# Kernel tuning notes

Measured on AMD Instinct MI355X. Metric: run time of the kernel, lower is better.

Reference implementation:

```python
import jax, jax.numpy as jnp
import numpy as np

P = 10      # num_prototypes == embed_dim
H = 2       # num_heads
F = 64      # ffn_dim
L = 2       # transformer_blocks
DH = P // H # head dim = 5


def _layernorm(x, g, b, eps=1e-5):
    mu = jnp.mean(x, axis=-1, keepdims=True)
    var = jnp.var(x, axis=-1, keepdims=True)
    return (x - mu) * jax.lax.rsqrt(var + eps) * g + b


def setup_inputs() -> dict:
    key = jax.random.key(0)
    ks = jax.random.split(key, 16)
    B = 1_000_000
    inp = {
        "x": jax.random.normal(ks[0], (B, 8), dtype=jnp.float32),
        "prototypes": jax.random.normal(ks[1], (P, 8), dtype=jnp.float32),
        # attention projections, stacked over layers
        "Wq": jax.random.normal(ks[2], (L, P, P), dtype=jnp.float32) * 0.1,
        "bq": jnp.zeros((L, P), dtype=jnp.float32),
        "Wk": jax.random.normal(ks[3], (L, P, P), dtype=jnp.float32) * 0.1,
        "bk": jnp.zeros((L, P), dtype=jnp.float32),
        "Wv": jax.random.normal(ks[4], (L, P, P), dtype=jnp.float32) * 0.1,
        "bv": jnp.zeros((L, P), dtype=jnp.float32),
        "Wo": jax.random.normal(ks[5], (L, P, P), dtype=jnp.float32) * 0.1,
        "bo": jnp.zeros((L, P), dtype=jnp.float32),
        "ln1_g": jnp.ones((L, P), dtype=jnp.float32),
        "ln1_b": jnp.zeros((L, P), dtype=jnp.float32),
        "ln2_g": jnp.ones((L, P), dtype=jnp.float32),
        "ln2_b": jnp.zeros((L, P), dtype=jnp.float32),
        # FFN
        "W1": jax.random.normal(ks[6], (L, P, F), dtype=jnp.float32) * 0.1,
        "b1": jnp.zeros((L, F), dtype=jnp.float32),
        "W2": jax.random.normal(ks[7], (L, F, P), dtype=jnp.float32) * 0.1,
        "b2": jnp.zeros((L, P), dtype=jnp.float32),
        # classifier (num_classes=2 -> single logit + sigmoid)
        "Wc": jax.random.normal(ks[8], (P, 1), dtype=jnp.float32) * 0.1,
        "bc": jnp.zeros((1,), dtype=jnp.float32),
    }
    return inp


def _forward(x, prototypes, Wq, bq, Wk, bk, Wv, bv, Wo, bo,
             ln1_g, ln1_b, ln2_g, ln2_b, W1, b1, W2, b2, Wc, bc):
    # ---- vectorized RBF kernel matrix (replaces the B*P python loop) ----
    x2 = jnp.sum(x * x, axis=-1, keepdims=True)            # [B,1]
    p2 = jnp.sum(prototypes * prototypes, axis=-1)          # [P]
    sq = x2 + p2[None, :] - 2.0 * (x @ prototypes.T)        # [B,P]
    km = jnp.exp(-sq)                                       # [B,P] quantum-kernel proxy

    seq = km[:, None, :]                                    # [B, S=1, P]
    scale = 1.0 / jnp.sqrt(jnp.asarray(DH, dtype=seq.dtype))
    B = seq.shape[0]

    for l in range(L):  # small fixed layer count
        # pre-norm multi-head self-attention (seq_len == 1)
        h = _layernorm(seq, ln1_g[l], ln1_b[l])
        q = (h @ Wq[l] + bq[l]).reshape(B, 1, H, DH)
        k = (h @ Wk[l] + bk[l]).reshape(B, 1, H, DH)
        v = (h @ Wv[l] + bv[l]).reshape(B, 1, H, DH)
        scores = jnp.einsum('bqhd,bkhd->bhqk', q, k) * scale
        attn = jax.nn.softmax(scores, axis=-1)
        o = jnp.einsum('bhqk,bkhd->bqhd', attn, v).reshape(B, 1, P)
        seq = seq + (o @ Wo[l] + bo[l])
        # pre-norm FFN
        h2 = _layernorm(seq, ln2_g[l], ln2_b[l])
        seq = seq + (jax.nn.gelu(h2 @ W1[l] + b1[l]) @ W2[l] + b2[l])

    logits = seq[:, 0, :] @ Wc + bc                          # [B,1]
    return jax.nn.sigmoid(logits)


def reference(x, prototypes, Wq, bq, Wk, bk, Wv, bv, Wo, bo,
              ln1_g, ln1_b, ln2_g, ln2_b, W1, b1, W2, b2, Wc, bc):
    return _forward(x, prototypes, Wq, bq, Wk, bk, Wv, bv, Wo, bo,
                    ln1_g, ln1_b, ln2_g, ln2_b, W1, b1, W2, b2, Wc, bc)
```

## Files before the change

### kernel.cpp

```cpp
#include <hip/hip_runtime.h>
#include <hip/hip_fp16.h>
#include <cmath>

#define PP 10
#define FF 64
#define LL 2
#define BLOCK 256
#define EPT 2
#define L2E 1.44269504088896f

typedef _Float16 h2 __attribute__((ext_vector_type(2)));

struct GeluCoef { float c[5]; };

#define WS_P2L   0
#define WS_MPROT 16
#define WS_M1P   96
#define WS_C1    196
#define WS_FFNU  216
#define WS_W2C   1752
#define WS_HC    1784

__device__ __forceinline__ float fast_sigmoid(float z) {
    return __builtin_amdgcn_rcpf(1.0f + exp2f(-L2E * z));
}

__device__ __forceinline__ unsigned int pack_h2f(float a, float b) {
    _Float16 ha = (_Float16)a, hb = (_Float16)b;
    unsigned short ua = __builtin_bit_cast(unsigned short, ha);
    unsigned short ub = __builtin_bit_cast(unsigned short, hb);
    return (unsigned int)ua | ((unsigned int)ub << 16);
}

__device__ __forceinline__ h2 h2bcast(float v) {
    _Float16 h = (_Float16)v;
    h2 r; r.x = h; r.y = h; return r;
}

__global__ __launch_bounds__(256) void prep_kernel(
    const float* __restrict__ protos,
    const float* __restrict__ Wv, const float* __restrict__ bv,
    const float* __restrict__ Wo, const float* __restrict__ bo,
    const float* __restrict__ ln1g, const float* __restrict__ ln1b,
    const float* __restrict__ ln2g, const float* __restrict__ ln2b,
    const float* __restrict__ W1, const float* __restrict__ b1,
    const float* __restrict__ W2, const float* __restrict__ b2,
    const float* __restrict__ Wc, const float* __restrict__ bc,
    float* __restrict__ ws)
{
    const int t = threadIdx.x;
    unsigned int* wsu = (unsigned int*)ws;
    if (t < PP) {
        float s = 0.0f;
        for (int k = 0; k < 8; ++k) { float v = protos[t * 8 + k]; s += v * v; }
        ws[WS_P2L + t] = L2E * s;
    }
    for (int idx = t; idx < PP * 8; idx += 256)
        ws[WS_MPROT + idx] = 2.0f * L2E * protos[idx];
    for (int idx = t; idx < LL * PP * 5; idx += 256) {
        int l = idx / (PP * 5);
        int r = idx % (PP * 5);
        int o = r / 5, jp = r % 5;
        float w[2];
        for (int d = 0; d < 2; ++d) {
            int j = 2 * jp + d;
            float s = 0.0f;
            for (int m = 0; m < PP; ++m)
                s += Wv[l * PP * PP + j * PP + m] * Wo[l * PP * PP + m * PP + o];
            w[d] = ln1g[l * PP + j] * s;
        }
        wsu[WS_M1P + idx] = pack_h2f(w[0], w[1]);
    }
    for (int idx = t; idx < LL * PP; idx += 256) {
        int l = idx / PP, o = idx % PP;
        float s = bo[l * PP + o];
        for (int m = 0; m < PP; ++m) s += bv[l * PP + m] * Wo[l * PP * PP + m * PP + o];
        for (int j = 0; j < PP; ++j) {
            float wv_wo = 0.0f;
            for (int m = 0; m < PP; ++m)
                wv_wo += Wv[l * PP * PP + j * PP + m] * Wo[l * PP * PP + m * PP + o];
            s += ln1b[l * PP + j] * wv_wo;
        }
        ws[WS_C1 + idx] = s;
    }
    for (int idx = t; idx < LL * (FF / 2) * 24; idx += 256) {
        int l = idx / ((FF / 2) * 24);
        int r = idx % ((FF / 2) * 24);
        int pr = r / 24, c = r % 24;
        int f0 = 2 * pr;
        unsigned int v = 0;
        if (c < 10) {
            int f = (c < 5) ? f0 : (f0 + 1);
            int jp = (c < 5) ? c : (c - 5);
            float wa = ln2g[l * PP + 2 * jp] * W1[l * PP * FF + (2 * jp) * FF + f];
            float wb = ln2g[l * PP + 2 * jp + 1] * W1[l * PP * FF + (2 * jp + 1) * FF + f];
            v = pack_h2f(wa, wb);
        } else if (c == 10 || c == 11) {
            int f = f0 + (c - 10);
            float s = b1[l * FF + f];
            for (int j = 0; j < PP; ++j)
                s += ln2b[l * PP + j] * W1[l * PP * FF + j * FF + f];
            v = __builtin_bit_cast(unsigned int, s);
        } else if (c < 22) {
            int o = c - 12;
            v = pack_h2f(W2[l * FF * PP + f0 * PP + o],
                         W2[l * FF * PP + (f0 + 1) * PP + o]);
        }
        wsu[WS_FFNU + idx] = v;
    }
    for (int idx = t; idx < FF / 2; idx += 256) {
        int f0 = 2 * idx;
        float a = 0.0f, b = 0.0f;
        for (int o = 0; o < PP; ++o) {
            a += W2[FF * PP + f0 * PP + o] * Wc[o];
            b += W2[FF * PP + (f0 + 1) * PP + o] * Wc[o];
        }
        wsu[WS_W2C + idx] = pack_h2f(a, b);
    }
    if (t == 0) {
        float s = bc[0];
        for (int o = 0; o < PP; ++o) s += Wc[o] * b2[PP + o];
        ws[WS_HC] = s;
    }
}

__device__ __forceinline__ void ln_onepass(const float* s, float* y) {
    float sum = 0.0f, sq = 0.0f;
#pragma unroll
    for (int j = 0; j < PP; ++j) { sum += s[j]; sq = fmaf(s[j], s[j], sq); }
    float mu = sum * 0.1f;
    float var = fmaf(-mu, mu, sq * 0.1f);
    float rs = __builtin_amdgcn_rsqf(var + 1e-5f);
    float mrs = -mu * rs;
#pragma unroll
    for (int j = 0; j < PP; ++j) y[j] = fmaf(s[j], rs, mrs);
}

__global__ __launch_bounds__(BLOCK) void hqcnn_kernel(
    const float* __restrict__ x,
    const float* __restrict__ b2,
    const float* __restrict__ Wc,
    const float* __restrict__ ws,
    float* __restrict__ out, int B, GeluCoef gc)
{
    const int t = threadIdx.x;
    const int base = blockIdx.x * (BLOCK * EPT) + t;
    const unsigned int* wsu = (const unsigned int*)ws;

    int idx[EPT];
    bool valid[EPT];
#pragma unroll
    for (int e = 0; e < EPT; ++e) {
        int i = base + e * BLOCK;
        valid[e] = (i < B);
        idx[e] = valid[e] ? i : (B - 1);
    }

    float xv[EPT][8];
#pragma unroll
    for (int e = 0; e < EPT; ++e) {
        const float4 a = ((const float4*)x)[idx[e] * 2];
        const float4 b = ((const float4*)x)[idx[e] * 2 + 1];
        xv[e][0]=a.x; xv[e][1]=a.y; xv[e][2]=a.z; xv[e][3]=a.w;
        xv[e][4]=b.x; xv[e][5]=b.y; xv[e][6]=b.z; xv[e][7]=b.w;
    }

    float xl[EPT];
#pragma unroll
    for (int e = 0; e < EPT; ++e) {
        float s = 0.0f;
#pragma unroll
        for (int k = 0; k < 8; ++k) s += xv[e][k] * xv[e][k];
        xl[e] = L2E * s;
    }
    float seq[EPT][PP];
#pragma unroll
    for (int p = 0; p < PP; ++p) {
        float p2l = ws[WS_P2L + p];
#pragma unroll
        for (int e = 0; e < EPT; ++e) {
            float s = -(xl[e] + p2l);
#pragma unroll
            for (int k = 0; k < 8; ++k) s += xv[e][k] * ws[WS_MPROT + p * 8 + k];
            seq[e][p] = exp2f(s);
        }
    }

    const h2 GC0 = h2bcast(gc.c[0]);
    const h2 GC1 = h2bcast(gc.c[1]);
    const h2 GC2 = h2bcast(gc.c[2]);
    const h2 GC3 = h2bcast(gc.c[3]);
    const h2 GC4 = h2bcast(gc.c[4]);
    const h2 HLF  = h2bcast(0.5f);

    float z[EPT];
#pragma unroll
    for (int e = 0; e < EPT; ++e) z[e] = 0.0f;

#pragma unroll
    for (int l = 0; l < LL; ++l) {
        float y[EPT][PP];
#pragma unroll
        for (int e = 0; e < EPT; ++e) ln_onepass(seq[e], y[e]);
        h2 y2a[EPT][5];
#pragma unroll
        for (int e = 0; e < EPT; ++e)
#pragma unroll
            for (int jp = 0; jp < 5; ++jp)
                y2a[e][jp] = __builtin_bit_cast(h2,
                    __floats2half2_rn(y[e][2 * jp], y[e][2 * jp + 1]));
        const unsigned int* m1p = wsu + WS_M1P + l * PP * 5;
#pragma unroll
        for (int o = 0; o < PP; ++o) {
            float c = ws[WS_C1 + l * PP + o];
            float a[EPT];
#pragma unroll
            for (int e = 0; e < EPT; ++e) a[e] = c;
#pragma unroll
            for (int jp = 0; jp < 5; ++jp) {
                h2 w = __builtin_bit_cast(h2, m1p[o * 5 + jp]);
#pragma unroll
                for (int e = 0; e < EPT; ++e)
                    a[e] = __builtin_amdgcn_fdot2(y2a[e][jp], w, a[e], false);
            }
#pragma unroll
            for (int e = 0; e < EPT; ++e) seq[e][o] += a[e];
        }
#pragma unroll
        for (int e = 0; e < EPT; ++e) ln_onepass(seq[e], y[e]);
        h2 y2[EPT][5];
#pragma unroll
        for (int e = 0; e < EPT; ++e)
#pragma unroll
            for (int jp = 0; jp < 5; ++jp)
                y2[e][jp] = __builtin_bit_cast(h2,
                    __floats2half2_rn(y[e][2 * jp], y[e][2 * jp + 1]));
        float acc[EPT][PP];
        if (l == 0) {
#pragma unroll
            for (int o = 0; o < PP; ++o) {
                float b = b2[o];
#pragma unroll
                for (int e = 0; e < EPT; ++e) acc[e][o] = b;
            }
        }
        const uint4* fw = (const uint4*)(wsu + WS_FFNU + l * (FF / 2) * 24);
#pragma unroll 1
        for (int sb = 0; sb < 4; ++sb) {
            const uint4* fsb = fw + sb * 8 * 6;
            h2 th[8][EPT];
#pragma unroll
            for (int p8 = 0; p8 < 8; ++p8) {
                const uint4* rec = fsb + p8 * 6;
                uint4 q0 = rec[0];
                uint4 q1 = rec[1];
                uint4 q2 = rec[2];
                h2 w1a[5], w1b[5];
                w1a[0] = __builtin_bit_cast(h2, q0.x);
                w1a[1] = __builtin_bit_cast(h2, q0.y);
                w1a[2] = __builtin_bit_cast(h2, q0.z);
                w1a[3] = __builtin_bit_cast(h2, q0.w);
                w1a[4] = __builtin_bit_cast(h2, q1.x);
                w1b[0] = __builtin_bit_cast(h2, q1.y);
                w1b[1] = __builtin_bit_cast(h2, q1.z);
                w1b[2] = __builtin_bit_cast(h2, q1.w);
                w1b[3] = __builtin_bit_cast(h2, q2.x);
                w1b[4] = __builtin_bit_cast(h2, q2.y);
                float bfa = __builtin_bit_cast(float, q2.z);
                float bfb = __builtin_bit_cast(float, q2.w);
                float ta[EPT], tb[EPT];
#pragma unroll
                for (int e = 0; e < EPT; ++e) { ta[e] = bfa; tb[e] = bfb; }
#pragma unroll
                for (int jp = 0; jp < 5; ++jp) {
#pragma unroll
                    for (int e = 0; e < EPT; ++e) {
                        ta[e] = __builtin_amdgcn_fdot2(y2[e][jp], w1a[jp], ta[e], false);
                        tb[e] = __builtin_amdgcn_fdot2(y2[e][jp], w1b[jp], tb[e], false);
                    }
                }
#pragma unroll
                for (int e = 0; e < EPT; ++e)
                    th[p8][e] = __builtin_bit_cast(h2, __floats2half2_rn(ta[e], tb[e]));
            }
#pragma unroll
            for (int p8 = 0; p8 < 8; ++p8) {
                h2 up[EPT];
#pragma unroll
                for (int e = 0; e < EPT; ++e) {
                    h2 X = th[p8][e];
                    h2 S = X * X;
                    h2 P = S * GC4 + GC3;
                    P = S * P + GC2;
                    P = S * P + GC1;
                    P = S * P + GC0;
                    h2 Hh = X * P + HLF;
                    up[e] = X * Hh;
                }
                if (l == 0) {
                    const uint4* rec = fsb + p8 * 6;
                    uint4 q3 = rec[3];
                    uint4 q4 = rec[4];
                    uint4 q5 = rec[5];
                    h2 w2p[PP];
                    w2p[0] = __builtin_bit_cast(h2, q3.x);
                    w2p[1] = __builtin_bit_cast(h2, q3.y);
                    w2p[2] = __builtin_bit_cast(h2, q3.z);
                    w2p[3] = __builtin_bit_cast(h2, q3.w);
                    w2p[4] = __builtin_bit_cast(h2, q4.x);
                    w2p[5] = __builtin_bit_cast(h2, q4.y);
                    w2p[6] = __builtin_bit_cast(h2, q4.z);
                    w2p[7] = __builtin_bit_cast(h2, q4.w);
                    w2p[8] = __builtin_bit_cast(h2, q5.x);
                    w2p[9] = __builtin_bit_cast(h2, q5.y);
#pragma unroll
                    for (int o = 0; o < PP; ++o) {
#pragma unroll
                        for (int e = 0; e < EPT; ++e)
                            acc[e][o] = __builtin_amdgcn_fdot2(up[e], w2p[o], acc[e][o], false);
                    }
                } else {
                    h2 wz = __builtin_bit_cast(h2, wsu[WS_W2C + sb * 8 + p8]);
#pragma unroll
                    for (int e = 0; e < EPT; ++e)
                        z[e] = __builtin_amdgcn_fdot2(up[e], wz, z[e], false);
                }
            }
        }
        if (l == 0) {
#pragma unroll
            for (int o = 0; o < PP; ++o) {
#pragma unroll
                for (int e = 0; e < EPT; ++e) seq[e][o] += acc[e][o];
            }
        }
    }

    float hc = ws[WS_HC];
#pragma unroll
    for (int e = 0; e < EPT; ++e) z[e] += hc;
#pragma unroll
    for (int o = 0; o < PP; ++o) {
        float w = Wc[o];
#pragma unroll
        for (int e = 0; e < EPT; ++e) z[e] += seq[e][o] * w;
    }
#pragma unroll
    for (int e = 0; e < EPT; ++e) {
        if (valid[e]) out[base + e * BLOCK] = fast_sigmoid(z[e]);
    }
}

extern "C" void kernel_launch(void* const* d_in, const int* in_sizes, int n_in,
                              void* d_out, int out_size, void* d_ws, size_t ws_size,
                              hipStream_t stream) {
    const float* x      = (const float*)d_in[0];
    const float* protos = (const float*)d_in[1];
    const float* Wv   = (const float*)d_in[6];
    const float* bv   = (const float*)d_in[7];
    const float* Wo   = (const float*)d_in[8];
    const float* bo   = (const float*)d_in[9];
    const float* ln1g = (const float*)d_in[10];
    const float* ln1b = (const float*)d_in[11];
    const float* ln2g = (const float*)d_in[12];
    const float* ln2b = (const float*)d_in[13];
    const float* W1   = (const float*)d_in[14];
    const float* b1   = (const float*)d_in[15];
    const float* W2   = (const float*)d_in[16];
    const float* b2   = (const float*)d_in[17];
    const float* Wc   = (const float*)d_in[18];
    const float* bc   = (const float*)d_in[19];
    float* out = (float*)d_out;
    float* ws  = (float*)d_ws;

    GeluCoef gcoef;
    {
        const double PI = 3.14159265358979323846;
        const double cc = 0.7978845608028654, aa = 0.044715;
        double sv[5], gd[5];
        for (int k = 0; k < 5; ++k) {
            double tk = 1.85 + 1.85 * std::cos((2 * k + 1) * PI / 10.0);
            sv[k] = tk * tk;
            gd[k] = std::tanh(cc * (tk + aa * tk * tk * tk)) / tk;
        }
        for (int j = 1; j < 5; ++j)
            for (int i = 4; i >= j; --i)
                gd[i] = (gd[i] - gd[i - 1]) / (sv[i] - sv[i - j]);
        double c[5] = {0, 0, 0, 0, 0};
        c[0] = gd[4];
        for (int k = 3; k >= 0; --k) {
            for (int i = 4; i >= 1; --i) c[i] = c[i - 1] - sv[k] * c[i];
            c[0] = -sv[k] * c[0] + gd[k];
        }
        for (int i = 0; i < 5; ++i) gcoef.c[i] = (float)(0.5 * c[i]);
    }

    prep_kernel<<<1, 256, 0, stream>>>(protos, Wv, bv, Wo, bo,
                                       ln1g, ln1b, ln2g, ln2b,
                                       W1, b1, W2, b2, Wc, bc, ws);

    const int B = in_sizes[0] / 8;
    const int grid = (B + BLOCK * EPT - 1) / (BLOCK * EPT);
    hqcnn_kernel<<<grid, BLOCK, 0, stream>>>(x, b2, Wc, ws, out, B, gcoef);
}
```

Measured before the change: 176.1 us.

## Move attention and FFN matmuls onto 16x16x16 fp16 MFMA with fragment-layout weights

Replaces the per-thread packed fdot2 evaluation of the folded attention and FFN with matrix-core MFMA instructions. Each wave handles 64 samples as four 16-column tiles, and weights are prepacked into MFMA A-fragment layout by the prep kernel. LayerNorm reductions become cross-lane shuffles because the feature dimension is spread over lanes. The RBF stage now reads prototypes directly. This frees VALU work in exchange for padding 10 features to 16 and adding shuffle overhead.

```diff
diff --git a/kernel.cpp b/kernel.cpp
--- a/kernel.cpp
+++ b/kernel.cpp
@@ -1,25 +1,23 @@
 #include <hip/hip_runtime.h>
-#include <hip/hip_fp16.h>
 #include <cmath>
 
 #define PP 10
 #define FF 64
 #define LL 2
 #define BLOCK 256
-#define EPT 2
 #define L2E 1.44269504088896f
 
+typedef float f32x4 __attribute__((ext_vector_type(4)));
+typedef _Float16 f16x4 __attribute__((ext_vector_type(4)));
 typedef _Float16 h2 __attribute__((ext_vector_type(2)));
 
 struct GeluCoef { float c[5]; };
 
-#define WS_P2L   0
-#define WS_MPROT 16
-#define WS_M1P   96
-#define WS_C1    196
-#define WS_FFNU  216
-#define WS_W2C   1752
-#define WS_HC    1784
+#define FB_B1 2304
+#define FB_C1 4352
+#define FB_B2 4864
+#define FB_WC 5120
+#define F_HC  5376
 
 __device__ __forceinline__ float fast_sigmoid(float z) {
     return __builtin_amdgcn_rcpf(1.0f + exp2f(-L2E * z));
@@ -37,8 +35,9 @@
     h2 r; r.x = h; r.y = h; return r;
 }
 
-__global__ __launch_bounds__(256) void prep_kernel(
-    const float* __restrict__ protos,
+#define MFMA(a, b, c) __builtin_amdgcn_mfma_f32_16x16x16f16((a), (b), (c), 0, 0, 0)
+
+__global__ __launch_bounds__(256) void prep2(
     const float* __restrict__ Wv, const float* __restrict__ bv,
     const float* __restrict__ Wo, const float* __restrict__ bo,
     const float* __restrict__ ln1g, const float* __restrict__ ln1b,
@@ -50,139 +49,200 @@
 {
     const int t = threadIdx.x;
     unsigned int* wsu = (unsigned int*)ws;
-    if (t < PP) {
-        float s = 0.0f;
-        for (int k = 0; k < 8; ++k) { float v = protos[t * 8 + k]; s += v * v; }
-        ws[WS_P2L + t] = L2E * s;
-    }
-    for (int idx = t; idx < PP * 8; idx += 256)
-        ws[WS_MPROT + idx] = 2.0f * L2E * protos[idx];
-    for (int idx = t; idx < LL * PP * 5; idx += 256) {
-        int l = idx / (PP * 5);
-        int r = idx % (PP * 5);
-        int o = r / 5, jp = r % 5;
-        float w[2];
-        for (int d = 0; d < 2; ++d) {
-            int j = 2 * jp + d;
-            float s = 0.0f;
-            for (int m = 0; m < PP; ++m)
-                s += Wv[l * PP * PP + j * PP + m] * Wo[l * PP * PP + m * PP + o];
-            w[d] = ln1g[l * PP + j] * s;
-        }
-        wsu[WS_M1P + idx] = pack_h2f(w[0], w[1]);
-    }
-    for (int idx = t; idx < LL * PP; idx += 256) {
-        int l = idx / PP, o = idx % PP;
-        float s = bo[l * PP + o];
-        for (int m = 0; m < PP; ++m) s += bv[l * PP + m] * Wo[l * PP * PP + m * PP + o];
-        for (int j = 0; j < PP; ++j) {
-            float wv_wo = 0.0f;
-            for (int m = 0; m < PP; ++m)
-                wv_wo += Wv[l * PP * PP + j * PP + m] * Wo[l * PP * PP + m * PP + o];
-            s += ln1b[l * PP + j] * wv_wo;
-        }
-        ws[WS_C1 + idx] = s;
-    }
-    for (int idx = t; idx < LL * (FF / 2) * 24; idx += 256) {
-        int l = idx / ((FF / 2) * 24);
-        int r = idx % ((FF / 2) * 24);
-        int pr = r / 24, c = r % 24;
-        int f0 = 2 * pr;
-        unsigned int v = 0;
-        if (c < 10) {
-            int f = (c < 5) ? f0 : (f0 + 1);
-            int jp = (c < 5) ? c : (c - 5);
-            float wa = ln2g[l * PP + 2 * jp] * W1[l * PP * FF + (2 * jp) * FF + f];
-            float wb = ln2g[l * PP + 2 * jp + 1] * W1[l * PP * FF + (2 * jp + 1) * FF + f];
-            v = pack_h2f(wa, wb);
-        } else if (c == 10 || c == 11) {
-            int f = f0 + (c - 10);
-            float s = b1[l * FF + f];
-            for (int j = 0; j < PP; ++j)
-                s += ln2b[l * PP + j] * W1[l * PP * FF + j * FF + f];
-            v = __builtin_bit_cast(unsigned int, s);
-        } else if (c < 22) {
-            int o = c - 12;
-            v = pack_h2f(W2[l * FF * PP + f0 * PP + o],
-                         W2[l * FF * PP + (f0 + 1) * PP + o]);
-        }
-        wsu[WS_FFNU + idx] = v;
-    }
-    for (int idx = t; idx < FF / 2; idx += 256) {
-        int f0 = 2 * idx;
-        float a = 0.0f, b = 0.0f;
-        for (int o = 0; o < PP; ++o) {
-            a += W2[FF * PP + f0 * PP + o] * Wc[o];
-            b += W2[FF * PP + (f0 + 1) * PP + o] * Wc[o];
-        }
-        wsu[WS_W2C + idx] = pack_h2f(a, b);
+
+    for (int idx = t; idx < 18 * 128; idx += 256) {
+        int F = idx >> 7, d = idx & 127;
+        int ln = d >> 1, half = d & 1;
+        int row = ln & 15;
+        int k0 = 4 * (ln >> 4) + 2 * half;
+        float v[2] = {0.0f, 0.0f};
+        if (F < 2) {
+            int l = F;
+            if (row < PP) {
+                for (int kk = 0; kk < 2; ++kk) {
+                    int j = k0 + kk;
+                    if (j < PP) {
+                        float s = 0.0f;
+                        for (int m = 0; m < PP; ++m)
+                            s += Wv[l*PP*PP + j*PP + m] * Wo[l*PP*PP + m*PP + row];
+                        v[kk] = ln1g[l*PP + j] * s;
+                    }
+                }
+            }
+        } else if (F < 10) {
+            int l = (F - 2) >> 2, m = (F - 2) & 3;
+            int f = 16 * m + row;
+            for (int kk = 0; kk < 2; ++kk) {
+                int j = k0 + kk;
+                if (j < PP) v[kk] = ln2g[l*PP + j] * W1[l*PP*FF + j*FF + f];
+            }
+        } else if (F < 14) {
+            int c = F - 10;
+            if (row < PP) {
+                for (int kk = 0; kk < 2; ++kk) {
+                    int f = 16 * c + k0 + kk;
+                    v[kk] = W2[f*PP + row];
+                }
+            }
+        } else {
+            int c = F - 14;
+            if (row == 0) {
+                for (int kk = 0; kk < 2; ++kk) {
+                    int f = 16 * c + k0 + kk;
+                    float s = 0.0f;
+                    for (int o = 0; o < PP; ++o) s += W2[FF*PP + f*PP + o] * Wc[o];
+                    v[kk] = s;
+                }
+            }
+        }
+        wsu[idx] = pack_h2f(v[0], v[1]);
+    }
+
+    for (int idx = t; idx < 2048; idx += 256) {
+        int lm = idx >> 8; int l = lm >> 2, m = lm & 3;
+        int r2 = idx & 255; int ln = r2 >> 2, rr = r2 & 3;
+        int f = 16 * m + 4 * (ln >> 4) + rr;
+        float s = b1[l*FF + f];
+        for (int j = 0; j < PP; ++j) s += ln2b[l*PP + j] * W1[l*PP*FF + j*FF + f];
+        ws[FB_B1 + idx] = s;
+    }
+
+    for (int idx = t; idx < 512; idx += 256) {
+        int l = idx >> 8;
+        int r2 = idx & 255; int ln = r2 >> 2, rr = r2 & 3;
+        int o = 4 * (ln >> 4) + rr;
+        float val = 0.0f;
+        if (o < PP) {
+            float s = bo[l*PP + o];
+            for (int m = 0; m < PP; ++m) s += bv[l*PP + m] * Wo[l*PP*PP + m*PP + o];
+            for (int j = 0; j < PP; ++j) {
+                float ww = 0.0f;
+                for (int m = 0; m < PP; ++m)
+                    ww += Wv[l*PP*PP + j*PP + m] * Wo[l*PP*PP + m*PP + o];
+                s += ln1b[l*PP + j] * ww;
+            }
+            val = s;
+        }
+        ws[FB_C1 + idx] = val;
+    }
+
+    if (t < 256) {
+        int ln = t >> 2, rr = t & 3;
+        int o = 4 * (ln >> 4) + rr;
+        ws[FB_B2 + t] = (o < PP) ? b2[o] : 0.0f;
+        ws[FB_WC + t] = (o < PP) ? Wc[o] : 0.0f;
     }
     if (t == 0) {
         float s = bc[0];
         for (int o = 0; o < PP; ++o) s += Wc[o] * b2[PP + o];
-        ws[WS_HC] = s;
-    }
-}
-
-__device__ __forceinline__ void ln_onepass(const float* s, float* y) {
-    float sum = 0.0f, sq = 0.0f;
-#pragma unroll
-    for (int j = 0; j < PP; ++j) { sum += s[j]; sq = fmaf(s[j], s[j], sq); }
-    float mu = sum * 0.1f;
-    float var = fmaf(-mu, mu, sq * 0.1f);
+        ws[F_HC] = s;
+    }
+}
+
+
+__device__ __forceinline__ f16x4 ln_pack(f32x4 s) {
+    float ls = (s.x + s.y) + (s.z + s.w);
+    float lq = fmaf(s.x, s.x, fmaf(s.y, s.y, fmaf(s.z, s.z, s.w * s.w)));
+    ls += __shfl_xor(ls, 16); ls += __shfl_xor(ls, 32);
+    lq += __shfl_xor(lq, 16); lq += __shfl_xor(lq, 32);
+    float mu = ls * 0.1f;
+    float var = fmaf(-mu, mu, lq * 0.1f);
     float rs = __builtin_amdgcn_rsqf(var + 1e-5f);
     float mrs = -mu * rs;
-#pragma unroll
-    for (int j = 0; j < PP; ++j) y[j] = fmaf(s[j], rs, mrs);
-}
-
-__global__ __launch_bounds__(BLOCK) void hqcnn_kernel(
-    const float* __restrict__ x,
-    const float* __restrict__ b2,
-    const float* __restrict__ Wc,
-    const float* __restrict__ ws,
-    float* __restrict__ out, int B, GeluCoef gc)
+    uint2 u;
+    u.x = pack_h2f(fmaf(s.x, rs, mrs), fmaf(s.y, rs, mrs));
+    u.y = pack_h2f(fmaf(s.z, rs, mrs), fmaf(s.w, rs, mrs));
+    return __builtin_bit_cast(f16x4, u);
+}
+
+__device__ __forceinline__ f16x4 gelu_pack(f32x4 tv, h2 G0, h2 G1, h2 G2, h2 G3,
+                                           h2 G4, h2 HLF) {
+    h2 X0 = __builtin_bit_cast(h2, pack_h2f(tv.x, tv.y));
+    h2 X1 = __builtin_bit_cast(h2, pack_h2f(tv.z, tv.w));
+    h2 S0 = X0 * X0, S1 = X1 * X1;
+    h2 P0 = S0 * G4 + G3, P1 = S1 * G4 + G3;
+    P0 = S0 * P0 + G2; P1 = S1 * P1 + G2;
+    P0 = S0 * P0 + G1; P1 = S1 * P1 + G1;
+    P0 = S0 * P0 + G0; P1 = S1 * P1 + G0;
+    h2 H0 = X0 * P0 + HLF, H1 = X1 * P1 + HLF;
+    h2 U0 = X0 * H0, U1 = X1 * H1;
+    uint2 u;
+    u.x = __builtin_bit_cast(unsigned int, U0);
+    u.y = __builtin_bit_cast(unsigned int, U1);
+    return __builtin_bit_cast(f16x4, u);
+}
+
+__global__ __launch_bounds__(BLOCK) void hq_mfma(
+    const float* __restrict__ x, const float* __restrict__ protos,
+    const float* __restrict__ ws, float* __restrict__ out, int B, GeluCoef gc)
 {
     const int t = threadIdx.x;
-    const int base = blockIdx.x * (BLOCK * EPT) + t;
-    const unsigned int* wsu = (const unsigned int*)ws;
-
-    int idx[EPT];
-    bool valid[EPT];
-#pragma unroll
-    for (int e = 0; e < EPT; ++e) {
-        int i = base + e * BLOCK;
-        valid[e] = (i < B);
-        idx[e] = valid[e] ? i : (B - 1);
-    }
-
-    float xv[EPT][8];
-#pragma unroll
-    for (int e = 0; e < EPT; ++e) {
-        const float4 a = ((const float4*)x)[idx[e] * 2];
-        const float4 b = ((const float4*)x)[idx[e] * 2 + 1];
-        xv[e][0]=a.x; xv[e][1]=a.y; xv[e][2]=a.z; xv[e][3]=a.w;
-        xv[e][4]=b.x; xv[e][5]=b.y; xv[e][6]=b.z; xv[e][7]=b.w;
-    }
-
-    float xl[EPT];
-#pragma unroll
-    for (int e = 0; e < EPT; ++e) {
-        float s = 0.0f;
-#pragma unroll
-        for (int k = 0; k < 8; ++k) s += xv[e][k] * xv[e][k];
-        xl[e] = L2E * s;
-    }
-    float seq[EPT][PP];
-#pragma unroll
-    for (int p = 0; p < PP; ++p) {
-        float p2l = ws[WS_P2L + p];
-#pragma unroll
-        for (int e = 0; e < EPT; ++e) {
-            float s = -(xl[e] + p2l);
-#pragma unroll
-            for (int k = 0; k < 8; ++k) s += xv[e][k] * ws[WS_MPROT + p * 8 + k];
-            seq[e][p] = exp2f(s);
+    const int lane = t & 63;
+    const int q = lane >> 4;
+    const int col = lane & 15;
+    const int wbase = blockIdx.x * BLOCK + (t >> 6) * 64;
+
+    const uint2* fr = (const uint2*)ws;
+    f16x4 aattn[2], affn1[2][4], affn2[4], aw2c[4];
+#pragma unroll
+    for (int l = 0; l < 2; ++l)
+        aattn[l] = __builtin_bit_cast(f16x4, fr[l * 64 + lane]);
+#pragma unroll
+    for (int l = 0; l < 2; ++l)
+#pragma unroll
+        for (int m = 0; m < 4; ++m)
+            affn1[l][m] = __builtin_bit_cast(f16x4, fr[(2 + l * 4 + m) * 64 + lane]);
+#pragma unroll
+    for (int c = 0; c < 4; ++c)
+        affn2[c] = __builtin_bit_cast(f16x4, fr[(10 + c) * 64 + lane]);
+#pragma unroll
+    for (int c = 0; c < 4; ++c)
+        aw2c[c] = __builtin_bit_cast(f16x4, fr[(14 + c) * 64 + lane]);
+
+    const f32x4* wv4 = (const f32x4*)ws;
+    f32x4 b1f[2][4], c1f[2];
+#pragma unroll
+    for (int l = 0; l < 2; ++l) {
+#pragma unroll
+        for (int m = 0; m < 4; ++m) b1f[l][m] = wv4[576 + (l * 4 + m) * 64 + lane];
+        c1f[l] = wv4[1088 + l * 64 + lane];
+    }
+    f32x4 b2f = wv4[1216 + lane];
+    f32x4 wcf = wv4[1280 + lane];
+    float hc = ws[F_HC];
+    f32x4 zi = {0.0f, 0.0f, 0.0f, 0.0f};
+    if (q == 0) zi.x = hc;
+
+    const float4* p4 = (const float4*)protos;
+    float mp2[4];
+#pragma unroll
+    for (int r = 0; r < 4; ++r) {
+        int p = 4 * q + r;
+        int pc = (p < PP) ? p : 0;
+        float4 a = p4[pc * 2], b = p4[pc * 2 + 1];
+        float s2 = a.x * a.x + a.y * a.y + a.z * a.z + a.w * a.w
+                 + b.x * b.x + b.y * b.y + b.z * b.z + b.w * b.w;
+        mp2[r] = (p < PP) ? (-L2E * s2) : -1e30f;
+    }
+
+    const float4* x4 = (const float4*)x;
+    f32x4 seq[4];
+#pragma unroll
+    for (int g = 0; g < 4; ++g) {
+        int e = wbase + g * 16 + col;
+        if (e >= B) e = B - 1;
+        float4 xa = x4[e * 2], xb = x4[e * 2 + 1];
+        float x2 = xa.x * xa.x + xa.y * xa.y + xa.z * xa.z + xa.w * xa.w
+                 + xb.x * xb.x + xb.y * xb.y + xb.z * xb.z + xb.w * xb.w;
+#pragma unroll
+        for (int r = 0; r < 4; ++r) {
+            int p = 4 * q + r;
+            int pc = (p < PP) ? p : 0;
+            float4 a = p4[pc * 2], b = p4[pc * 2 + 1];
+            float dot = xa.x * a.x + xa.y * a.y + xa.z * a.z + xa.w * a.w
+                      + xb.x * b.x + xb.y * b.y + xb.z * b.z + xb.w * b.w;
+            float s = fmaf(2.0f * L2E, dot, fmaf(-L2E, x2, mp2[r]));
+            seq[g][r] = exp2f(s);
         }
     }
 
@@ -191,163 +251,55 @@
     const h2 GC2 = h2bcast(gc.c[2]);
     const h2 GC3 = h2bcast(gc.c[3]);
     const h2 GC4 = h2bcast(gc.c[4]);
-    const h2 HLF  = h2bcast(0.5f);
-
-    float z[EPT];
-#pragma unroll
-    for (int e = 0; e < EPT; ++e) z[e] = 0.0f;
-
-#pragma unroll
-    for (int l = 0; l < LL; ++l) {
-        float y[EPT][PP];
-#pragma unroll
-        for (int e = 0; e < EPT; ++e) ln_onepass(seq[e], y[e]);
-        h2 y2a[EPT][5];
-#pragma unroll
-        for (int e = 0; e < EPT; ++e)
-#pragma unroll
-            for (int jp = 0; jp < 5; ++jp)
-                y2a[e][jp] = __builtin_bit_cast(h2,
-                    __floats2half2_rn(y[e][2 * jp], y[e][2 * jp + 1]));
-        const unsigned int* m1p = wsu + WS_M1P + l * PP * 5;
-#pragma unroll
-        for (int o = 0; o < PP; ++o) {
-            float c = ws[WS_C1 + l * PP + o];
-            float a[EPT];
-#pragma unroll
-            for (int e = 0; e < EPT; ++e) a[e] = c;
-#pragma unroll
-            for (int jp = 0; jp < 5; ++jp) {
-                h2 w = __builtin_bit_cast(h2, m1p[o * 5 + jp]);
-#pragma unroll
-                for (int e = 0; e < EPT; ++e)
-                    a[e] = __builtin_amdgcn_fdot2(y2a[e][jp], w, a[e], false);
-            }
-#pragma unroll
-            for (int e = 0; e < EPT; ++e) seq[e][o] += a[e];
-        }
-#pragma unroll
-        for (int e = 0; e < EPT; ++e) ln_onepass(seq[e], y[e]);
-        h2 y2[EPT][5];
-#pragma unroll
-        for (int e = 0; e < EPT; ++e)
-#pragma unroll
-            for (int jp = 0; jp < 5; ++jp)
-                y2[e][jp] = __builtin_bit_cast(h2,
-                    __floats2half2_rn(y[e][2 * jp], y[e][2 * jp + 1]));
-        float acc[EPT][PP];
+    const h2 HLF = h2bcast(0.5f);
+
+#pragma unroll
+    for (int l = 0; l < 2; ++l) {
+#pragma unroll
+        for (int g = 0; g < 4; ++g) {
+            f16x4 y = ln_pack(seq[g]);
+            f32x4 d = MFMA(aattn[l], y, c1f[l]);
+            seq[g] += d;
+        }
         if (l == 0) {
 #pragma unroll
-            for (int o = 0; o < PP; ++o) {
-                float b = b2[o];
-#pragma unroll
-                for (int e = 0; e < EPT; ++e) acc[e][o] = b;
-            }
-        }
-        const uint4* fw = (const uint4*)(wsu + WS_FFNU + l * (FF / 2) * 24);
-#pragma unroll 1
-        for (int sb = 0; sb < 4; ++sb) {
-            const uint4* fsb = fw + sb * 8 * 6;
-            h2 th[8][EPT];
-#pragma unroll
-            for (int p8 = 0; p8 < 8; ++p8) {
-                const uint4* rec = fsb + p8 * 6;
-                uint4 q0 = rec[0];
-                uint4 q1 = rec[1];
-                uint4 q2 = rec[2];
-                h2 w1a[5], w1b[5];
-                w1a[0] = __builtin_bit_cast(h2, q0.x);
-                w1a[1] = __builtin_bit_cast(h2, q0.y);
-                w1a[2] = __builtin_bit_cast(h2, q0.z);
-                w1a[3] = __builtin_bit_cast(h2, q0.w);
-                w1a[4] = __builtin_bit_cast(h2, q1.x);
-                w1b[0] = __builtin_bit_cast(h2, q1.y);
-                w1b[1] = __builtin_bit_cast(h2, q1.z);
-                w1b[2] = __builtin_bit_cast(h2, q1.w);
-                w1b[3] = __builtin_bit_cast(h2, q2.x);
-                w1b[4] = __builtin_bit_cast(h2, q2.y);
-                float bfa = __builtin_bit_cast(float, q2.z);
-                float bfb = __builtin_bit_cast(float, q2.w);
-                float ta[EPT], tb[EPT];
-#pragma unroll
-                for (int e = 0; e < EPT; ++e) { ta[e] = bfa; tb[e] = bfb; }
-#pragma unroll
-                for (int jp = 0; jp < 5; ++jp) {
-#pragma unroll
-                    for (int e = 0; e < EPT; ++e) {
-                        ta[e] = __builtin_amdgcn_fdot2(y2[e][jp], w1a[jp], ta[e], false);
-                        tb[e] = __builtin_amdgcn_fdot2(y2[e][jp], w1b[jp], tb[e], false);
-                    }
+            for (int g = 0; g < 4; ++g) {
+                f16x4 y = ln_pack(seq[g]);
+                f16x4 u0 = gelu_pack(MFMA(affn1[0][0], y, b1f[0][0]), GC0, GC1, GC2, GC3, GC4, HLF);
+                f16x4 u1 = gelu_pack(MFMA(affn1[0][1], y, b1f[0][1]), GC0, GC1, GC2, GC3, GC4, HLF);
+                f16x4 u2 = gelu_pack(MFMA(affn1[0][2], y, b1f[0][2]), GC0, GC1, GC2, GC3, GC4, HLF);
+                f16x4 u3 = gelu_pack(MFMA(affn1[0][3], y, b1f[0][3]), GC0, GC1, GC2, GC3, GC4, HLF);
+                f32x4 o2 = MFMA(affn2[0], u0, b2f);
+                o2 = MFMA(affn2[1], u1, o2);
+                o2 = MFMA(affn2[2], u2, o2);
+                o2 = MFMA(affn2[3], u3, o2);
+                seq[g] += o2;
+            }
+        } else {
+#pragma unroll
+            for (int g = 0; g < 4; ++g) {
+                f16x4 y = ln_pack(seq[g]);
+                f16x4 u0 = gelu_pack(MFMA(affn1[1][0], y, b1f[1][0]), GC0, GC1, GC2, GC3, GC4, HLF);
+                f16x4 u1 = gelu_pack(MFMA(affn1[1][1], y, b1f[1][1]), GC0, GC1, GC2, GC3, GC4, HLF);
+                f16x4 u2 = gelu_pack(MFMA(affn1[1][2], y, b1f[1][2]), GC0, GC1, GC2, GC3, GC4, HLF);
+                f16x4 u3 = gelu_pack(MFMA(affn1[1][3], y, b1f[1][3]), GC0, GC1, GC2, GC3, GC4, HLF);
+                f32x4 zc = MFMA(aw2c[0], u0, zi);
+                zc = MFMA(aw2c[1], u1, zc);
+                zc = MFMA(aw2c[2], u2, zc);
+                zc = MFMA(aw2c[3], u3, zc);
+                float wcs = fmaf(wcf.x, seq[g].x,
+                            fmaf(wcf.y, seq[g].y,
+                            fmaf(wcf.z, seq[g].z, wcf.w * seq[g].w)));
+                wcs += __shfl_xor(wcs, 16);
+                wcs += __shfl_xor(wcs, 32);
+                float z = wcs + zc.x;
+                float r = fast_sigmoid(z);
+                if (q == 0) {
+                    int e0 = wbase + g * 16 + col;
+                    if (e0 < B) out[e0] = r;
                 }
-#pragma unroll
-                for (int e = 0; e < EPT; ++e)
-                    th[p8][e] = __builtin_bit_cast(h2, __floats2half2_rn(ta[e], tb[e]));
-            }
-#pragma unroll
-            for (int p8 = 0; p8 < 8; ++p8) {
-                h2 up[EPT];
-#pragma unroll
-                for (int e = 0; e < EPT; ++e) {
-                    h2 X = th[p8][e];
-                    h2 S = X * X;
-                    h2 P = S * GC4 + GC3;
-                    P = S * P + GC2;
-                    P = S * P + GC1;
-                    P = S * P + GC0;
-                    h2 Hh = X * P + HLF;
-                    up[e] = X * Hh;
-                }
-                if (l == 0) {
-                    const uint4* rec = fsb + p8 * 6;
-                    uint4 q3 = rec[3];
-                    uint4 q4 = rec[4];
-                    uint4 q5 = rec[5];
-                    h2 w2p[PP];
-                    w2p[0] = __builtin_bit_cast(h2, q3.x);
-                    w2p[1] = __builtin_bit_cast(h2, q3.y);
-                    w2p[2] = __builtin_bit_cast(h2, q3.z);
-                    w2p[3] = __builtin_bit_cast(h2, q3.w);
-                    w2p[4] = __builtin_bit_cast(h2, q4.x);
-                    w2p[5] = __builtin_bit_cast(h2, q4.y);
-                    w2p[6] = __builtin_bit_cast(h2, q4.z);
-                    w2p[7] = __builtin_bit_cast(h2, q4.w);
-                    w2p[8] = __builtin_bit_cast(h2, q5.x);
-                    w2p[9] = __builtin_bit_cast(h2, q5.y);
-#pragma unroll
-                    for (int o = 0; o < PP; ++o) {
-#pragma unroll
-                        for (int e = 0; e < EPT; ++e)
-                            acc[e][o] = __builtin_amdgcn_fdot2(up[e], w2p[o], acc[e][o], false);
-                    }
-                } else {
-                    h2 wz = __builtin_bit_cast(h2, wsu[WS_W2C + sb * 8 + p8]);
-#pragma unroll
-                    for (int e = 0; e < EPT; ++e)
-                        z[e] = __builtin_amdgcn_fdot2(up[e], wz, z[e], false);
-                }
-            }
-        }
-        if (l == 0) {
-#pragma unroll
-            for (int o = 0; o < PP; ++o) {
-#pragma unroll
-                for (int e = 0; e < EPT; ++e) seq[e][o] += acc[e][o];
-            }
-        }
-    }
-
-    float hc = ws[WS_HC];
-#pragma unroll
-    for (int e = 0; e < EPT; ++e) z[e] += hc;
-#pragma unroll
-    for (int o = 0; o < PP; ++o) {
-        float w = Wc[o];
-#pragma unroll
-        for (int e = 0; e < EPT; ++e) z[e] += seq[e][o] * w;
-    }
-#pragma unroll
-    for (int e = 0; e < EPT; ++e) {
-        if (valid[e]) out[base + e * BLOCK] = fast_sigmoid(z[e]);
+            }
+        }
     }
 }
 
@@ -395,11 +347,10 @@
         for (int i = 0; i < 5; ++i) gcoef.c[i] = (float)(0.5 * c[i]);
     }
 
-    prep_kernel<<<1, 256, 0, stream>>>(protos, Wv, bv, Wo, bo,
-                                       ln1g, ln1b, ln2g, ln2b,
-                                       W1, b1, W2, b2, Wc, bc, ws);
+    prep2<<<1, 256, 0, stream>>>(Wv, bv, Wo, bo, ln1g, ln1b, ln2g, ln2b,
+                                 W1, b1, W2, b2, Wc, bc, ws);
 
     const int B = in_sizes[0] / 8;
-    const int grid = (B + BLOCK * EPT - 1) / (BLOCK * EPT);
-    hqcnn_kernel<<<grid, BLOCK, 0, stream>>>(x, b2, Wc, ws, out, B, gcoef);
-}
+    const int grid = (B + BLOCK - 1) / BLOCK;
+    hq_mfma<<<grid, BLOCK, 0, stream>>>(x, protos, ws, out, B, gcoef);
+}
```

Measured after the change: 177.6 us. Within noise of the previous version (+0.9%).
